# Kernel tuning notes

Hardware: AMD Instinct MI355X
Metric: run time of the kernel (lower is better)

The kernel has to match this reference:

```python
import jax, jax.numpy as jnp
import numpy as np

B, S, D = 32, 2048, 768   # batch, seq_len, hidden_dim
NL, NF = 512, 64          # num_lines, num_functions


def setup_inputs() -> dict:
    key = jax.random.key(0)
    k = jax.random.split(key, 4)
    hidden_states = jax.random.normal(k[0], (B, S, D), dtype=jnp.float32)
    proj_W = jax.random.normal(k[1], (D, D), dtype=jnp.float32) * 0.02
    proj_b = jnp.zeros((D,), dtype=jnp.float32)
    # start <= end per pair, indices in-range
    line_boundaries = jnp.sort(jax.random.randint(k[2], (B, NL, 2), 0, S), axis=-1)
    function_boundaries = jnp.sort(jax.random.randint(k[3], (B, NF, 2), 0, NL), axis=-1)
    return dict(hidden_states=hidden_states, proj_W=proj_W, proj_b=proj_b,
                line_boundaries=line_boundaries, function_boundaries=function_boundaries)


def segment_mean(x, boundaries):
    """Mean of x[b, start:end] per segment; zeros when start >= end.
    x: [B, S, D]; boundaries: [B, N, 2] -> [B, N, D].
    Uses an exclusive prefix-sum so all segments are reduced in one pass."""
    csum = jnp.concatenate([jnp.zeros_like(x[:, :1]), jnp.cumsum(x, axis=1)], axis=1)  # [B, S+1, D]
    start = boundaries[..., 0]
    end = boundaries[..., 1]
    take = lambda idx: jnp.take_along_axis(csum, idx[..., None], axis=1)  # [B, N, D]
    seg_sum = take(end) - take(start)
    length = (end - start).astype(x.dtype)[..., None]
    return jnp.where(length > 0, seg_sum / jnp.maximum(length, 1.0), jnp.zeros_like(seg_sum))


def reference(hidden_states, proj_W, proj_b, line_boundaries, function_boundaries):
    # CodeEncoder projection of pretrained hidden states (no complexity features)
    token_emb = hidden_states @ proj_W + proj_b                     # [B, S, D]
    # _encode_lines: per-boundary token mean
    line_emb = segment_mean(token_emb, line_boundaries)             # [B, NL, D]
    # _encode_functions: per-boundary line mean
    func_emb = segment_mean(line_emb, function_boundaries)          # [B, NF, D]
    # AdaptiveAvgPool1d(1) over the function axis
    file_emb = jnp.mean(func_emb, axis=1)                           # [B, D]
    return token_emb, line_emb, func_emb, file_emb
```

## Files before the change

### kernel.cpp

```cpp
#include <hip/hip_runtime.h>
#include <hip/hip_bf16.h>

#define Bq 32
#define Sq 2048
#define Dq 768
#define NLq 512
#define NFq 64

typedef unsigned short u16;
typedef __attribute__((ext_vector_type(4))) unsigned short us4;
typedef __attribute__((ext_vector_type(8))) unsigned short us8;
typedef __attribute__((ext_vector_type(8))) short s16x8;
typedef __attribute__((ext_vector_type(4))) float f32x4;

static __device__ __forceinline__ u16 f2bf(float f) {
  unsigned int u = __builtin_bit_cast(unsigned int, f);
  u += 0x7fffu + ((u >> 16) & 1u);
  return (u16)(u >> 16);
}

__global__ __launch_bounds__(256) void wt_kernel(const float* __restrict__ W,
                                                 u16* __restrict__ Wt) {
  int idx = blockIdx.x * 256 + threadIdx.x;
  int n = idx / Dq, k = idx % Dq;
  Wt[idx] = f2bf(W[(size_t)k * Dq + n]);
}

__global__ __launch_bounds__(256) void gemm_kernel(const float* __restrict__ A,
                                                   const u16* __restrict__ Wt,
                                                   const float* __restrict__ bias,
                                                   float* __restrict__ C) {
  __shared__ u16 As[128 * 32];
  __shared__ u16 Bs[128 * 32];
  const int tid = threadIdx.x;
  const int gn0 = blockIdx.x * 128;
  const int gm0 = blockIdx.y * 128;
  const int wave = tid >> 6, lane = tid & 63;
  const int lm = lane & 15, quad = lane >> 4;
  const int wm = (wave & 1) * 64, wn = (wave >> 1) * 64;
  const int ar = tid >> 3, aq = tid & 7;
  const int bn = tid >> 2, bc = tid & 3;

  f32x4 acc[4][4] = {};

  for (int k0 = 0; k0 < Dq; k0 += 32) {
#pragma unroll
    for (int p = 0; p < 4; ++p) {
      const int row = p * 32 + ar;
      const float4 v = *(const float4*)(A + (size_t)(gm0 + row) * Dq + k0 + aq * 4);
      us4 o;
      o.x = f2bf(v.x); o.y = f2bf(v.y); o.z = f2bf(v.z); o.w = f2bf(v.w);
      *(us4*)&As[row * 32 + aq * 4] = o;
    }
#pragma unroll
    for (int p = 0; p < 2; ++p) {
      const int row = p * 64 + bn;
      const us8 v = *(const us8*)(Wt + (size_t)(gn0 + row) * Dq + k0 + bc * 8);
      *(us8*)&Bs[row * 32 + bc * 8] = v;
    }
    __syncthreads();

    s16x8 af[4], bfr[4];
#pragma unroll
    for (int i = 0; i < 4; ++i)
      af[i] = *(const s16x8*)&As[(wm + i * 16 + lm) * 32 + quad * 8];
#pragma unroll
    for (int i = 0; i < 4; ++i)
      bfr[i] = *(const s16x8*)&Bs[(wn + i * 16 + lm) * 32 + quad * 8];
#pragma unroll
    for (int mi = 0; mi < 4; ++mi)
#pragma unroll
      for (int ni = 0; ni < 4; ++ni)
        acc[mi][ni] = __builtin_amdgcn_mfma_f32_16x16x32_bf16(af[mi], bfr[ni],
                                                              acc[mi][ni], 0, 0, 0);
    __syncthreads();
  }

#pragma unroll
  for (int ni = 0; ni < 4; ++ni) {
    const int gn = gn0 + wn + ni * 16 + lm;
    const float bv = bias[gn];
#pragma unroll
    for (int mi = 0; mi < 4; ++mi) {
#pragma unroll
      for (int r = 0; r < 4; ++r) {
        const int gm = gm0 + wm + mi * 16 + quad * 4 + r;
        C[(size_t)gm * Dq + gn] = acc[mi][ni][r] + bv;
      }
    }
  }
}

__global__ __launch_bounds__(64) void csum_kernel(const float* __restrict__ tok,
                                                  float* __restrict__ csum) {
  const int blk = blockIdx.x;
  const int b = blk / 12;
  const int d = (blk % 12) * 64 + threadIdx.x;
  const float* src = tok + (size_t)b * Sq * Dq + d;
  float* dst = csum + (size_t)b * (Sq + 1) * Dq + d;
  dst[0] = 0.f;
  float run = 0.f;
  for (int s0 = 0; s0 < Sq; s0 += 16) {
    float v[16];
#pragma unroll
    for (int i = 0; i < 16; ++i) v[i] = src[(size_t)(s0 + i) * Dq];
#pragma unroll
    for (int i = 0; i < 16; ++i) {
      run += v[i];
      dst[(size_t)(s0 + i + 1) * Dq] = run;
    }
  }
}

__global__ __launch_bounds__(64) void line_kernel(const float* __restrict__ csum,
                                                  const int* __restrict__ lb,
                                                  float* __restrict__ lemb,
                                                  float* __restrict__ lcsum) {
  __shared__ int sb[NLq * 2];
  const int tid = threadIdx.x;
  const int blk = blockIdx.x;
  const int b = blk / 12;
  const int d = (blk % 12) * 64 + tid;
  const int4* lb4 = (const int4*)(lb + (size_t)b * NLq * 2);
#pragma unroll
  for (int i = tid; i < NLq * 2 / 4; i += 64) ((int4*)sb)[i] = lb4[i];
  __syncthreads();

  const float* cs = csum + (size_t)b * (Sq + 1) * Dq + d;
  float* le = lemb + (size_t)b * NLq * Dq + d;
  float* lc = lcsum + (size_t)b * (NLq + 1) * Dq + d;
  lc[0] = 0.f;
  float run = 0.f;
  for (int n0 = 0; n0 < NLq; n0 += 8) {
    float ve[8], vs[8];
    int len[8];
#pragma unroll
    for (int i = 0; i < 8; ++i) {
      const int s0 = sb[2 * (n0 + i)], s1 = sb[2 * (n0 + i) + 1];
      len[i] = s1 - s0;
      vs[i] = cs[(size_t)s0 * Dq];
      ve[i] = cs[(size_t)s1 * Dq];
    }
#pragma unroll
    for (int i = 0; i < 8; ++i) {
      const float v = len[i] > 0 ? (ve[i] - vs[i]) / (float)len[i] : 0.f;
      le[(size_t)(n0 + i) * Dq] = v;
      run += v;
      lc[(size_t)(n0 + i + 1) * Dq] = run;
    }
  }
}

__global__ __launch_bounds__(64) void func_kernel(const float* __restrict__ lcsum,
                                                  const int* __restrict__ fb,
                                                  float* __restrict__ femb,
                                                  float* __restrict__ file) {
  __shared__ int sb[NFq * 2];
  const int tid = threadIdx.x;
  const int blk = blockIdx.x;
  const int b = blk / 12;
  const int d = (blk % 12) * 64 + tid;
  if (tid < NFq * 2 / 4) ((int4*)sb)[tid] = ((const int4*)(fb + (size_t)b * NFq * 2))[tid];
  __syncthreads();

  const float* lc = lcsum + (size_t)b * (NLq + 1) * Dq + d;
  float* fe = femb + (size_t)b * NFq * Dq + d;
  float acc = 0.f;
#pragma unroll 8
  for (int f = 0; f < NFq; ++f) {
    const int l0 = sb[2 * f], l1 = sb[2 * f + 1];
    const float v = l1 > l0 ? (lc[(size_t)l1 * Dq] - lc[(size_t)l0 * Dq]) / (float)(l1 - l0)
                            : 0.f;
    fe[(size_t)f * Dq] = v;
    acc += v;
  }
  file[(size_t)b * Dq + d] = acc * (1.f / (float)NFq);
}

extern "C" void kernel_launch(void* const* d_in, const int* in_sizes, int n_in,
                              void* d_out, int out_size, void* d_ws, size_t ws_size,
                              hipStream_t stream) {
  const float* hs   = (const float*)d_in[0];
  const float* W    = (const float*)d_in[1];
  const float* bias = (const float*)d_in[2];
  const int* lb     = (const int*)d_in[3];
  const int* fb     = (const int*)d_in[4];

  float* out = (float*)d_out;
  float* token = out;
  float* line  = token + (size_t)Bq * Sq * Dq;
  float* func  = line + (size_t)Bq * NLq * Dq;
  float* file  = func + (size_t)Bq * NFq * Dq;

  float* csum  = (float*)d_ws;
  float* lcsum = csum + (size_t)Bq * (Sq + 1) * Dq;
  u16* Wt      = (u16*)(lcsum + (size_t)Bq * (NLq + 1) * Dq);

  wt_kernel<<<(Dq * Dq) / 256, 256, 0, stream>>>(W, Wt);
  gemm_kernel<<<dim3(Dq / 128, (Bq * Sq) / 128), 256, 0, stream>>>(hs, Wt, bias, token);
  csum_kernel<<<Bq * (Dq / 64), 64, 0, stream>>>(token, csum);
  line_kernel<<<Bq * (Dq / 64), 64, 0, stream>>>(csum, lb, line, lcsum);
  func_kernel<<<Bq * (Dq / 64), 64, 0, stream>>>(lcsum, fb, func, file);
}
```

Measured before the change: 793.0 us.

## Chunk prefix scans with GEMM-fused partial sums and LDS-direct bf16 GEMM loads

Hidden states are first converted to bf16 in a separate pass, and the GEMM then loads A and B tiles straight into LDS with global_load_lds. The GEMM epilogue also writes per-128-row column sums. The serial token and line cumsums, which ran on only 384 blocks of 64 threads, become chunked scans: a small scan over the chunk partials followed by parallel per-chunk scans. This exposes far more parallelism in the scan stages. In exchange it adds extra kernels and a full bf16 copy of the activations, and the workspace buffers are aliased in a way that depends on the launch order.

```diff
diff --git a/kernel.cpp b/kernel.cpp
--- a/kernel.cpp
+++ b/kernel.cpp
@@ -6,10 +6,11 @@
 #define Dq 768
 #define NLq 512
 #define NFq 64
+#define SCHUNKS 16
+#define LCHUNKS 8
 
 typedef unsigned short u16;
 typedef __attribute__((ext_vector_type(4))) unsigned short us4;
-typedef __attribute__((ext_vector_type(8))) unsigned short us8;
 typedef __attribute__((ext_vector_type(8))) short s16x8;
 typedef __attribute__((ext_vector_type(4))) float f32x4;
 
@@ -17,6 +18,21 @@
   unsigned int u = __builtin_bit_cast(unsigned int, f);
   u += 0x7fffu + ((u >> 16) & 1u);
   return (u16)(u >> 16);
+}
+
+static __device__ __forceinline__ void gload16(const void* g, void* l) {
+  __builtin_amdgcn_global_load_lds(
+      (const __attribute__((address_space(1))) unsigned int*)g,
+      (__attribute__((address_space(3))) unsigned int*)l, 16, 0, 0);
+}
+
+__global__ __launch_bounds__(256) void cvta_kernel(const float* __restrict__ hs,
+                                                   u16* __restrict__ Abf) {
+  const size_t i = (size_t)blockIdx.x * 256 + threadIdx.x;
+  const float4 v = ((const float4*)hs)[i];
+  us4 o;
+  o.x = f2bf(v.x); o.y = f2bf(v.y); o.z = f2bf(v.z); o.w = f2bf(v.w);
+  ((us4*)Abf)[i] = o;
 }
 
 __global__ __launch_bounds__(256) void wt_kernel(const float* __restrict__ W,
@@ -26,38 +42,37 @@
   Wt[idx] = f2bf(W[(size_t)k * Dq + n]);
 }
 
-__global__ __launch_bounds__(256) void gemm_kernel(const float* __restrict__ A,
+__global__ __launch_bounds__(256) void gemm_kernel(const u16* __restrict__ Abf,
                                                    const u16* __restrict__ Wt,
                                                    const float* __restrict__ bias,
-                                                   float* __restrict__ C) {
+                                                   float* __restrict__ C,
+                                                   float* __restrict__ part16) {
   __shared__ u16 As[128 * 32];
   __shared__ u16 Bs[128 * 32];
+  __shared__ float ps[2][128];
   const int tid = threadIdx.x;
   const int gn0 = blockIdx.x * 128;
   const int gm0 = blockIdx.y * 128;
   const int wave = tid >> 6, lane = tid & 63;
   const int lm = lane & 15, quad = lane >> 4;
   const int wm = (wave & 1) * 64, wn = (wave >> 1) * 64;
-  const int ar = tid >> 3, aq = tid & 7;
-  const int bn = tid >> 2, bc = tid & 3;
+
+  const char* ga0 = (const char*)Abf + (size_t)(gm0 + (tid >> 2)) * (Dq * 2) + (tid & 3) * 16;
+  const char* ga1 = ga0 + (size_t)64 * (Dq * 2);
+  const char* gb0 = (const char*)Wt + (size_t)(gn0 + (tid >> 2)) * (Dq * 2) + (tid & 3) * 16;
+  const char* gb1 = gb0 + (size_t)64 * (Dq * 2);
+  char* lA = (char*)As + wave * 1024;
+  char* lB = (char*)Bs + wave * 1024;
 
   f32x4 acc[4][4] = {};
 
-  for (int k0 = 0; k0 < Dq; k0 += 32) {
-#pragma unroll
-    for (int p = 0; p < 4; ++p) {
-      const int row = p * 32 + ar;
-      const float4 v = *(const float4*)(A + (size_t)(gm0 + row) * Dq + k0 + aq * 4);
-      us4 o;
-      o.x = f2bf(v.x); o.y = f2bf(v.y); o.z = f2bf(v.z); o.w = f2bf(v.w);
-      *(us4*)&As[row * 32 + aq * 4] = o;
-    }
-#pragma unroll
-    for (int p = 0; p < 2; ++p) {
-      const int row = p * 64 + bn;
-      const us8 v = *(const us8*)(Wt + (size_t)(gn0 + row) * Dq + k0 + bc * 8);
-      *(us8*)&Bs[row * 32 + bc * 8] = v;
-    }
+  for (int kk = 0; kk < Dq / 32; ++kk) {
+    __syncthreads();
+    gload16(ga0, lA);
+    gload16(ga1, lA + 4096);
+    gload16(gb0, lB);
+    gload16(gb1, lB + 4096);
+    ga0 += 64; ga1 += 64; gb0 += 64; gb1 += 64;
     __syncthreads();
 
     s16x8 af[4], bfr[4];
@@ -73,41 +88,64 @@
       for (int ni = 0; ni < 4; ++ni)
         acc[mi][ni] = __builtin_amdgcn_mfma_f32_16x16x32_bf16(af[mi], bfr[ni],
                                                               acc[mi][ni], 0, 0, 0);
-    __syncthreads();
   }
 
 #pragma unroll
   for (int ni = 0; ni < 4; ++ni) {
     const int gn = gn0 + wn + ni * 16 + lm;
     const float bv = bias[gn];
+    float psum = 0.f;
 #pragma unroll
     for (int mi = 0; mi < 4; ++mi) {
 #pragma unroll
       for (int r = 0; r < 4; ++r) {
         const int gm = gm0 + wm + mi * 16 + quad * 4 + r;
-        C[(size_t)gm * Dq + gn] = acc[mi][ni][r] + bv;
+        const float cv = acc[mi][ni][r] + bv;
+        C[(size_t)gm * Dq + gn] = cv;
+        psum += cv;
       }
     }
-  }
-}
-
-__global__ __launch_bounds__(64) void csum_kernel(const float* __restrict__ tok,
-                                                  float* __restrict__ csum) {
-  const int blk = blockIdx.x;
-  const int b = blk / 12;
-  const int d = (blk % 12) * 64 + threadIdx.x;
-  const float* src = tok + (size_t)b * Sq * Dq + d;
-  float* dst = csum + (size_t)b * (Sq + 1) * Dq + d;
-  dst[0] = 0.f;
+    psum += __shfl_xor(psum, 16);
+    psum += __shfl_xor(psum, 32);
+    if (lane < 16) ps[wave & 1][wn + ni * 16 + lm] = psum;
+  }
+  __syncthreads();
+  if (tid < 128) {
+    const int b = gm0 >> 11;
+    const int sc = (gm0 >> 7) & 15;
+    part16[((size_t)b * SCHUNKS + sc) * Dq + gn0 + tid] = ps[0][tid] + ps[1][tid];
+  }
+}
+
+__global__ __launch_bounds__(256) void scan_kernel(float* __restrict__ p, int C) {
+  const int idx = blockIdx.x * 256 + threadIdx.x;
+  const int b = idx / Dq, d = idx % Dq;
   float run = 0.f;
-  for (int s0 = 0; s0 < Sq; s0 += 16) {
-    float v[16];
-#pragma unroll
-    for (int i = 0; i < 16; ++i) v[i] = src[(size_t)(s0 + i) * Dq];
-#pragma unroll
-    for (int i = 0; i < 16; ++i) {
+  for (int c = 0; c < C; ++c) {
+    const size_t o = ((size_t)b * C + c) * Dq + d;
+    const float v = p[o];
+    p[o] = run;
+    run += v;
+  }
+}
+
+__global__ __launch_bounds__(256) void csum_kernel(const float* __restrict__ tok,
+                                                   const float* __restrict__ part16,
+                                                   float* __restrict__ csum) {
+  const int sc = blockIdx.x, dc = blockIdx.y, b = blockIdx.z;
+  const int d = dc * 256 + threadIdx.x;
+  const float* src = tok + ((size_t)b * Sq + sc * 128) * Dq + d;
+  float* dst = csum + ((size_t)b * (Sq + 1) + sc * 128 + 1) * Dq + d;
+  float run = part16[((size_t)b * SCHUNKS + sc) * Dq + d];
+  if (sc == 0) csum[(size_t)b * (Sq + 1) * Dq + d] = 0.f;
+  for (int s0 = 0; s0 < 128; s0 += 8) {
+    float v[8];
+#pragma unroll
+    for (int i = 0; i < 8; ++i) v[i] = src[(size_t)(s0 + i) * Dq];
+#pragma unroll
+    for (int i = 0; i < 8; ++i) {
       run += v[i];
-      dst[(size_t)(s0 + i + 1) * Dq] = run;
+      dst[(size_t)(s0 + i) * Dq] = run;
     }
   }
 }
@@ -115,24 +153,19 @@
 __global__ __launch_bounds__(64) void line_kernel(const float* __restrict__ csum,
                                                   const int* __restrict__ lb,
                                                   float* __restrict__ lemb,
-                                                  float* __restrict__ lcsum) {
-  __shared__ int sb[NLq * 2];
+                                                  float* __restrict__ lpart) {
+  __shared__ int sb[128];
+  const int lc = blockIdx.x, d64 = blockIdx.y, b = blockIdx.z;
   const int tid = threadIdx.x;
-  const int blk = blockIdx.x;
-  const int b = blk / 12;
-  const int d = (blk % 12) * 64 + tid;
-  const int4* lb4 = (const int4*)(lb + (size_t)b * NLq * 2);
-#pragma unroll
-  for (int i = tid; i < NLq * 2 / 4; i += 64) ((int4*)sb)[i] = lb4[i];
+  if (tid < 32)
+    ((int4*)sb)[tid] = ((const int4*)(lb + ((size_t)b * NLq + lc * 64) * 2))[tid];
   __syncthreads();
-
+  const int d = d64 * 64 + tid;
   const float* cs = csum + (size_t)b * (Sq + 1) * Dq + d;
-  float* le = lemb + (size_t)b * NLq * Dq + d;
-  float* lc = lcsum + (size_t)b * (NLq + 1) * Dq + d;
-  lc[0] = 0.f;
-  float run = 0.f;
-  for (int n0 = 0; n0 < NLq; n0 += 8) {
-    float ve[8], vs[8];
+  float* le = lemb + ((size_t)b * NLq + lc * 64) * Dq + d;
+  float sum = 0.f;
+  for (int n0 = 0; n0 < 64; n0 += 8) {
+    float vs[8], ve[8];
     int len[8];
 #pragma unroll
     for (int i = 0; i < 8; ++i) {
@@ -145,8 +178,29 @@
     for (int i = 0; i < 8; ++i) {
       const float v = len[i] > 0 ? (ve[i] - vs[i]) / (float)len[i] : 0.f;
       le[(size_t)(n0 + i) * Dq] = v;
-      run += v;
-      lc[(size_t)(n0 + i + 1) * Dq] = run;
+      sum += v;
+    }
+  }
+  lpart[((size_t)b * LCHUNKS + lc) * Dq + d] = sum;
+}
+
+__global__ __launch_bounds__(256) void lcsum_kernel(const float* __restrict__ lemb,
+                                                    const float* __restrict__ lpart,
+                                                    float* __restrict__ lcsum) {
+  const int lc = blockIdx.x, dc = blockIdx.y, b = blockIdx.z;
+  const int d = dc * 256 + threadIdx.x;
+  const float* src = lemb + ((size_t)b * NLq + lc * 64) * Dq + d;
+  float* dst = lcsum + ((size_t)b * (NLq + 1) + lc * 64 + 1) * Dq + d;
+  float run = lpart[((size_t)b * LCHUNKS + lc) * Dq + d];
+  if (lc == 0) lcsum[(size_t)b * (NLq + 1) * Dq + d] = 0.f;
+  for (int n0 = 0; n0 < 64; n0 += 8) {
+    float v[8];
+#pragma unroll
+    for (int i = 0; i < 8; ++i) v[i] = src[(size_t)(n0 + i) * Dq];
+#pragma unroll
+    for (int i = 0; i < 8; ++i) {
+      run += v[i];
+      dst[(size_t)(n0 + i) * Dq] = run;
     }
   }
 }
@@ -157,12 +211,11 @@
                                                   float* __restrict__ file) {
   __shared__ int sb[NFq * 2];
   const int tid = threadIdx.x;
-  const int blk = blockIdx.x;
-  const int b = blk / 12;
-  const int d = (blk % 12) * 64 + tid;
-  if (tid < NFq * 2 / 4) ((int4*)sb)[tid] = ((const int4*)(fb + (size_t)b * NFq * 2))[tid];
+  const int d64 = blockIdx.x, b = blockIdx.y;
+  const int d = d64 * 64 + tid;
+  if (tid < NFq * 2 / 4)
+    ((int4*)sb)[tid] = ((const int4*)(fb + (size_t)b * NFq * 2))[tid];
   __syncthreads();
-
   const float* lc = lcsum + (size_t)b * (NLq + 1) * Dq + d;
   float* fe = femb + (size_t)b * NFq * Dq + d;
   float acc = 0.f;
@@ -192,13 +245,21 @@
   float* func  = line + (size_t)Bq * NLq * Dq;
   float* file  = func + (size_t)Bq * NFq * Dq;
 
-  float* csum  = (float*)d_ws;
-  float* lcsum = csum + (size_t)Bq * (Sq + 1) * Dq;
-  u16* Wt      = (u16*)(lcsum + (size_t)Bq * (NLq + 1) * Dq);
-
+  char* ws = (char*)d_ws;
+  float* csum   = (float*)ws;
+  u16*   Abf    = (u16*)ws;
+  float* lcsum  = (float*)(ws + 201498624);
+  float* part16 = lcsum;
+  u16*   Wt     = (u16*)(ws + 201498624 + 50442240);
+  float* lpart  = (float*)Wt;
+
+  cvta_kernel<<<(Bq * Sq * Dq / 4) / 256, 256, 0, stream>>>(hs, Abf);
   wt_kernel<<<(Dq * Dq) / 256, 256, 0, stream>>>(W, Wt);
-  gemm_kernel<<<dim3(Dq / 128, (Bq * Sq) / 128), 256, 0, stream>>>(hs, Wt, bias, token);
-  csum_kernel<<<Bq * (Dq / 64), 64, 0, stream>>>(token, csum);
-  line_kernel<<<Bq * (Dq / 64), 64, 0, stream>>>(csum, lb, line, lcsum);
-  func_kernel<<<Bq * (Dq / 64), 64, 0, stream>>>(lcsum, fb, func, file);
-}
+  gemm_kernel<<<dim3(Dq / 128, (Bq * Sq) / 128), 256, 0, stream>>>(Abf, Wt, bias, token, part16);
+  scan_kernel<<<(Bq * Dq) / 256, 256, 0, stream>>>(part16, SCHUNKS);
+  csum_kernel<<<dim3(SCHUNKS, 3, Bq), 256, 0, stream>>>(token, part16, csum);
+  line_kernel<<<dim3(LCHUNKS, 12, Bq), 64, 0, stream>>>(csum, lb, line, lpart);
+  scan_kernel<<<(Bq * Dq) / 256, 256, 0, stream>>>(lpart, LCHUNKS);
+  lcsum_kernel<<<dim3(LCHUNKS, 3, Bq), 256, 0, stream>>>(line, lpart, lcsum);
+  func_kernel<<<dim3(12, Bq), 64, 0, stream>>>(lcsum, fb, func, file);
+}
```

Measured after the change: 676.8 us. 1.17x faster.
